# Optimization experiments

Hardware: AMD Instinct MI355X
Metric: run time of the kernel (lower is better)

The kernel has to match this reference:

```python
import jax, jax.numpy as jnp
import numpy as np

K = 3          # kernel_size
PAD = 1        # padding
FOCAL = 50.0
DMIN = 1.0
DMAX = 50.0
ORIG_H = 512.0  # original_image_size[1]


def setup_inputs() -> dict:
    key = jax.random.key(0)
    k1, k2 = jax.random.split(key)
    x = jax.random.normal(k1, (4, 64, 256, 256), dtype=jnp.float32)
    # conv weight [out_ch, in_ch, K, K] (bias=False)
    W = jax.random.normal(k2, (64, 64, K, K), dtype=jnp.float32) * 0.05
    return {"x": x, "W": W}


def _bilinear(img, xs, ys):
    """Bilinear sample img [B,C,H,W] at float pixel coords xs, ys [B,Ho,Wo].
    Zero padding outside the image (grid_sample semantics)."""
    B, C, H, Wd = img.shape
    Ho, Wo = xs.shape[1], xs.shape[2]
    x0 = jnp.floor(xs); y0 = jnp.floor(ys)
    wx1 = xs - x0; wx0 = 1.0 - wx1
    wy1 = ys - y0; wy0 = 1.0 - wy1
    img_flat = img.reshape(B, C, H * Wd)

    def gat(ix, iy):
        ixi = ix.astype(jnp.int32); iyi = iy.astype(jnp.int32)
        valid = (ixi >= 0) & (ixi < Wd) & (iyi >= 0) & (iyi < H)
        idx = jnp.clip(iyi, 0, H - 1) * Wd + jnp.clip(ixi, 0, Wd - 1)
        v = jnp.take_along_axis(img_flat, idx.reshape(B, 1, Ho * Wo), axis=2)
        v = v.reshape(B, C, Ho, Wo)
        return v * valid[:, None].astype(img.dtype)

    return (gat(x0, y0) * (wx0 * wy0)[:, None]
            + gat(x0 + 1, y0) * (wx1 * wy0)[:, None]
            + gat(x0, y0 + 1) * (wx0 * wy1)[:, None]
            + gat(x0 + 1, y0 + 1) * (wx1 * wy1)[:, None])


def reference(x, W):
    B, C, H, Wd = x.shape
    downsample = ORIG_H / H  # 2.0 for H=256

    # upper branch: plain 3x3 conv, padding 1, no bias
    x_upper = jax.lax.conv_general_dilated(x, W, (1, 1), [(PAD, PAD), (PAD, PAD)])

    # geometry -> clamped depth (geometry_method='max', formulation='depth')
    depth = jnp.clip(jnp.max(x, axis=1), DMIN, DMAX)  # [B,H,W]

    # Frontal homography: Hom01 = I with [1,2] = focal/(downsample*depth);
    # its inverse Hom10 shifts y by -s.
    s = FOCAL / (downsample * depth)  # [B,H,W]

    xi = jnp.arange(Wd, dtype=x.dtype)[None, None, :]
    yi = jnp.arange(H, dtype=x.dtype)[None, :, None]
    xs = jnp.broadcast_to(xi, (B, H, Wd))
    ys = yi - s  # Hom10 applied to pixel coords

    # warp input with per-pixel Hom10 (pass_warped_images=True)
    x2 = _bilinear(x, xs, ys)

    # deformable conv: per-pixel offset from Hom10 is (dx,dy)=(0,-s) for all 9 taps
    x_lower = jnp.zeros_like(x_upper)
    for ky in range(K):
        for kx in range(K):
            sx = xs + (kx - PAD)
            sy = ys + (ky - PAD)
            tap = _bilinear(x2, sx, sy)  # [B,C,H,W]
            x_lower = x_lower + jnp.einsum('bchw,oc->bohw', tap, W[:, :, ky, kx])

    # project with 'min' over the stacked (upper, lower) branches
    return jnp.minimum(x_upper, x_lower)
```

## Files before the change

### kernel.cpp

```cpp
#include <hip/hip_runtime.h>
#include <cmath>

constexpr int BB = 4, CC = 64, HH = 256, WW = 256;
constexpr int WP = 258;
constexpr int C2R = 257;

typedef short short8 __attribute__((ext_vector_type(8)));
typedef float f32x4 __attribute__((ext_vector_type(4)));
#define MFMA_BF16 __builtin_amdgcn_mfma_f32_16x16x32_bf16

union U16x8 { uint4 v; unsigned short h[8]; };
union U16x4 { uint2 v; unsigned short h[4]; };

__device__ inline unsigned short f2bf(float f) {
  unsigned u = __builtin_bit_cast(unsigned, f);
  u += 0x7fffu + ((u >> 16) & 1u);
  return (unsigned short)(u >> 16);
}
__device__ inline unsigned short f2bf_trunc(float f) {
  return (unsigned short)(__builtin_bit_cast(unsigned, f) >> 16);
}
__device__ inline float bf2f(unsigned short h) {
  unsigned u = ((unsigned)h) << 16;
  return __builtin_bit_cast(float, u);
}

__global__ __launch_bounds__(256, 4) void k_pack(const float* __restrict__ x,
                                                 float* __restrict__ s,
                                                 unsigned short* __restrict__ xn) {
  __shared__ float tile[CC * 129];
  __shared__ float pmax[2][128];
  const int t = threadIdx.x;
  const int half = blockIdx.x & 1, y = blockIdx.x >> 1, b = blockIdx.y;
  const int px0 = half * 128;
  const int pxl = t & 127, chb = (t >> 7) * 32;

  const float* base = x + (size_t)b * CC * HH * WW + (size_t)y * WW + px0 + pxl;
  float m = -1e30f;
#pragma unroll 8
  for (int i = 0; i < 32; ++i) {
    float v = base[(size_t)(chb + i) * HH * WW];
    tile[(chb + i) * 129 + pxl] = v;
    m = fmaxf(m, v);
  }
  pmax[t >> 7][pxl] = m;

  uint4* xn4 = (uint4*)xn;
  if (t < 8) {
    int col = half ? (WP - 1) : 0;
    xn4[(((size_t)(b * HH + y) * WP + col) * CC + t * 8) >> 3] =
        make_uint4(0, 0, 0, 0);
  }
  __syncthreads();

  if (t < 128) {
    float mm = fmaxf(pmax[0][t], pmax[1][t]);
    s[(b * HH + y) * WW + px0 + t] = 25.0f / fminf(fmaxf(mm, 1.0f), 50.0f);
  }
#pragma unroll
  for (int g = 0; g < 4; ++g) {
    int px = g * 32 + (t >> 3), c8 = t & 7;
    U16x8 r;
#pragma unroll
    for (int j = 0; j < 8; ++j) r.h[j] = f2bf(tile[(c8 * 8 + j) * 129 + px]);
    xn4[(((size_t)(b * HH + y) * WP + px0 + px + 1) * CC + c8 * 8) >> 3] = r.v;
  }
}

__global__ __launch_bounds__(256) void k_wpack(const float* __restrict__ Wt,
                                               unsigned short* __restrict__ Wp) {
  int gid = blockIdx.x * 256 + threadIdx.x;
  int lane = gid & 63, kc = (gid >> 6) & 1, mt = (gid >> 7) & 3, tap = gid >> 9;
  int o = mt * 16 + (lane & 15);
  int kb = kc * 32 + (lane >> 4) * 8;
  int ky = tap / 3, kx = tap % 3;
  U16x8 r;
#pragma unroll
  for (int j = 0; j < 8; ++j)
    r.h[j] = f2bf(Wt[o * 576 + (kb + j) * 9 + ky * 3 + kx]);
  ((uint4*)Wp)[gid] = r.v;
}

__global__ __launch_bounds__(256, 4) void k_lower(const unsigned short* __restrict__ xn,
                                                  const unsigned short* __restrict__ Wp,
                                                  const float* __restrict__ s,
                                                  unsigned short* __restrict__ c2) {
  __shared__ uint4 lds[2112];
  const int t = threadIdx.x;
  const int ctile = blockIdx.x & 3, tr = blockIdx.x >> 2;
  const int b = blockIdx.y;
  const int r0 = tr * 2 - 1;
  const int colBase = ctile * 64;

  const uint4* xn4 = (const uint4*)xn;
#pragma unroll 1
  for (int g = 0; g < 3; ++g) {
    float w0a[3], w1a[3];
    int o0a[3], o1a[3], la[3];
    bool act[3], va[3];
#pragma unroll
    for (int j = 0; j < 3; ++j) {
      int idx = (g * 3 + j) * 256 + t;
      act[j] = idx < 2112;
      int rr_ = idx / 528, rem = idx % 528;
      int col_ = rem >> 3, ch_ = rem & 7;
      int xrow = r0 - 1 + rr_;
      va[j] = act[j] && (xrow >= 0) && (xrow < HH);
      la[j] = (rr_ * 66 + col_) * 8 + (ch_ ^ (col_ & 7));
      float sv = 0.0f;
      int pxc = min(max(colBase + col_ - 1, 0), WW - 1);
      if (va[j]) sv = s[(b * HH + min(max(xrow, 0), HH - 1)) * WW + pxc];
      float ys = (float)xrow - sv;
      float fy = floorf(ys);
      float wfr = ys - fy;
      int i0 = (int)fy;
      w0a[j] = (i0 >= 0) ? 1.0f - wfr : 0.0f;
      w1a[j] = (i0 + 1 >= 0) ? wfr : 0.0f;
      int a0 = min(max(i0, 0), HH - 1), a1 = min(max(i0 + 1, 0), HH - 1);
      o0a[j] = ((b * HH + a0) * WP + colBase + col_) * 8 + ch_;
      o1a[j] = ((b * HH + a1) * WP + colBase + col_) * 8 + ch_;
    }
#pragma unroll
    for (int j = 0; j < 3; ++j) {
      if (act[j]) {
        uint4 v = make_uint4(0, 0, 0, 0);
        if (va[j]) {
          U16x8 u0, u1, rr;
          u0.v = xn4[o0a[j]];
          u1.v = xn4[o1a[j]];
#pragma unroll
          for (int k = 0; k < 8; ++k)
            rr.h[k] = f2bf_trunc(w0a[j] * bf2f(u0.h[k]) + w1a[j] * bf2f(u1.h[k]));
          v = rr.v;
        }
        lds[la[j]] = v;
      }
    }
  }

  const int lane = t & 63, w = t >> 6;
  const int ow = w & 1, ch2 = w >> 1;
  const int quad = lane >> 4, l15 = lane & 15;
  const uint4* wp4 = (const uint4*)Wp;
  __syncthreads();

  f32x4 acc[2][2][2];
#pragma unroll
  for (int pt = 0; pt < 2; ++pt)
#pragma unroll
    for (int rr = 0; rr < 2; ++rr)
#pragma unroll
      for (int ct = 0; ct < 2; ++ct) acc[pt][rr][ct] = {0.f, 0.f, 0.f, 0.f};

#pragma unroll 1
  for (int kc = 0; kc < 2; ++kc) {
    short8 wf[9][2];
#pragma unroll
    for (int tap = 0; tap < 9; ++tap)
#pragma unroll
      for (int ct = 0; ct < 2; ++ct)
        wf[tap][ct] = __builtin_bit_cast(
            short8, wp4[((tap * 4 + (ow * 2 + ct)) * 2 + kc) * 64 + lane]);
#pragma unroll
    for (int pt = 0; pt < 2; ++pt) {
#pragma unroll
      for (int ir = 0; ir < 4; ++ir) {
#pragma unroll
        for (int kx = 0; kx < 3; ++kx) {
          int col = ch2 * 32 + pt * 16 + l15 + kx;
          short8 xf = __builtin_bit_cast(
              short8, lds[(ir * 66 + col) * 8 + ((kc * 4 + quad) ^ (col & 7))]);
          if (ir <= 2) {
#pragma unroll
            for (int ct = 0; ct < 2; ++ct)
              acc[pt][0][ct] = MFMA_BF16(wf[ir * 3 + kx][ct], xf, acc[pt][0][ct], 0, 0, 0);
          }
          if (ir >= 1) {
#pragma unroll
            for (int ct = 0; ct < 2; ++ct)
              acc[pt][1][ct] = MFMA_BF16(wf[(ir - 1) * 3 + kx][ct], xf, acc[pt][1][ct], 0, 0, 0);
          }
        }
      }
    }
  }

  uint2* c2u = (uint2*)c2;
#pragma unroll
  for (int pt = 0; pt < 2; ++pt) {
    int px = colBase + ch2 * 32 + pt * 16 + l15;
#pragma unroll
    for (int rr = 0; rr < 2; ++rr) {
      int r = r0 + rr;
      if (r > 255) continue;
#pragma unroll
      for (int ct = 0; ct < 2; ++ct) {
        f32x4 A = acc[pt][rr][ct];
        int og = (ow * 2 + ct) * 4 + quad;
        unsigned short h0 = f2bf(A[0]), h1 = f2bf(A[1]), h2 = f2bf(A[2]), h3 = f2bf(A[3]);
        uint2 val = make_uint2((unsigned)h0 | ((unsigned)h1 << 16),
                               (unsigned)h2 | ((unsigned)h3 << 16));
        c2u[(size_t)((b * 16 + og) * C2R + (r + 1)) * WW + px] = val;
      }
    }
  }
}

__global__ __launch_bounds__(256, 4) void k_final(const unsigned short* __restrict__ xn,
                                                  const unsigned short* __restrict__ Wp,
                                                  const float* __restrict__ s,
                                                  const unsigned short* __restrict__ c2,
                                                  float* __restrict__ out) {
  __shared__ uint4 lds[2112];
  const int t = threadIdx.x;
  const int ctile = blockIdx.x & 3, tr = blockIdx.x >> 2;
  const int b = blockIdx.y;
  const int y0 = tr * 2;
  const int colBase = ctile * 64;

  const uint4* src4 = (const uint4*)xn;
#pragma unroll 1
  for (int i = 0; i < 9; ++i) {
    int idx = i * 256 + t;
    if (idx < 2112) {
      int rr_ = idx / 528, rem = idx % 528;
      int col_ = rem >> 3, ch_ = rem & 7;
      int xrow = y0 - 1 + rr_;
      uint4 v = make_uint4(0, 0, 0, 0);
      if (xrow >= 0 && xrow < HH)
        v = src4[((size_t)(b * HH + xrow) * WP + colBase + col_) * 8 + ch_];
      lds[(rr_ * 66 + col_) * 8 + (ch_ ^ (col_ & 7))] = v;
    }
  }

  const int lane = t & 63, w = t >> 6;
  const int ow = w & 1, ch2 = w >> 1;
  const int quad = lane >> 4, l15 = lane & 15;
  const uint4* wp4 = (const uint4*)Wp;
  __syncthreads();

  f32x4 acc[2][2][2];
#pragma unroll
  for (int pt = 0; pt < 2; ++pt)
#pragma unroll
    for (int rr = 0; rr < 2; ++rr)
#pragma unroll
      for (int ct = 0; ct < 2; ++ct) acc[pt][rr][ct] = {0.f, 0.f, 0.f, 0.f};

#pragma unroll 1
  for (int kc = 0; kc < 2; ++kc) {
    short8 wf[9][2];
#pragma unroll
    for (int tap = 0; tap < 9; ++tap)
#pragma unroll
      for (int ct = 0; ct < 2; ++ct)
        wf[tap][ct] = __builtin_bit_cast(
            short8, wp4[((tap * 4 + (ow * 2 + ct)) * 2 + kc) * 64 + lane]);
#pragma unroll
    for (int pt = 0; pt < 2; ++pt) {
#pragma unroll
      for (int ir = 0; ir < 4; ++ir) {
#pragma unroll
        for (int kx = 0; kx < 3; ++kx) {
          int col = ch2 * 32 + pt * 16 + l15 + kx;
          short8 xf = __builtin_bit_cast(
              short8, lds[(ir * 66 + col) * 8 + ((kc * 4 + quad) ^ (col & 7))]);
          if (ir <= 2) {
#pragma unroll
            for (int ct = 0; ct < 2; ++ct)
              acc[pt][0][ct] = MFMA_BF16(wf[ir * 3 + kx][ct], xf, acc[pt][0][ct], 0, 0, 0);
          }
          if (ir >= 1) {
#pragma unroll
            for (int ct = 0; ct < 2; ++ct)
              acc[pt][1][ct] = MFMA_BF16(wf[(ir - 1) * 3 + kx][ct], xf, acc[pt][1][ct], 0, 0, 0);
          }
        }
      }
    }
  }

  const uint2* c2u = (const uint2*)c2;
#pragma unroll
  for (int pt = 0; pt < 2; ++pt) {
    int px = colBase + ch2 * 32 + pt * 16 + l15;
#pragma unroll
    for (int rr = 0; rr < 2; ++rr) {
      int y = y0 + rr;
      float sv = s[(b * HH + y) * WW + px];
      float ys = (float)y - sv;
      float fy = floorf(ys);
      float wfr = ys - fy;
      int i0 = (int)fy;
      float lw0 = (i0 + 1 >= 0 && i0 + 1 <= HH) ? 1.0f - wfr : 0.0f;
      float lw1 = (i0 + 2 >= 0 && i0 + 2 <= HH) ? wfr : 0.0f;
      int a0 = min(max(i0 + 1, 0), HH);
      int a1 = min(max(i0 + 2, 0), HH);
#pragma unroll
      for (int ct = 0; ct < 2; ++ct) {
        f32x4 A = acc[pt][rr][ct];
        int og = (ow * 2 + ct) * 4 + quad;
        U16x4 v0, v1;
        v0.v = c2u[(size_t)((b * 16 + og) * C2R + a0) * WW + px];
        v1.v = c2u[(size_t)((b * 16 + og) * C2R + a1) * WW + px];
#pragma unroll
        for (int reg = 0; reg < 4; ++reg) {
          float lower = lw0 * bf2f(v0.h[reg]) + lw1 * bf2f(v1.h[reg]);
          out[((size_t)(b * CC + og * 4 + reg) * HH + y) * WW + px] =
              fminf(A[reg], lower);
        }
      }
    }
  }
}

extern "C" void kernel_launch(void* const* d_in, const int* in_sizes, int n_in,
                              void* d_out, int out_size, void* d_ws, size_t ws_size,
                              hipStream_t stream) {
  const float* x = (const float*)d_in[0];
  const float* Wt = (const float*)d_in[1];
  float* out = (float*)d_out;

  char* ws = (char*)d_ws;
  float* s = (float*)ws;
  unsigned short* Wp = (unsigned short*)(ws + 1048576);
  unsigned short* xn = (unsigned short*)(ws + 1122304);
  unsigned short* c2 = (unsigned short*)(ws + 34938880);
  k_pack<<<dim3(HH * 2, BB), 256, 0, stream>>>(x, s, xn);
  k_wpack<<<dim3(18), 256, 0, stream>>>(Wt, Wp);
  k_lower<<<dim3(4 * 129, BB), 256, 0, stream>>>(xn, Wp, s, c2);
  k_final<<<dim3(4 * 128, BB), 256, 0, stream>>>(xn, Wp, s, c2, out);
}
```

Measured before the change: 190.2 us.

## Fuse four kernels into one persistent kernel with software grid barriers

Merges the pack, weight-pack, lower-branch and final kernels into a single persistent launch of 1024 blocks. Stages are separated by atomic-counter grid barriers, and each block loops over tiles for the conv stages. This removes per-kernel launch gaps and tail effects. In exchange it adds a memset and spin-wait barriers, and it relies on all 1024 blocks being co-resident (4 per CU on 256 CUs); if they are not, it will hang or hit the barrier timeout.

```diff
diff --git a/kernel.cpp b/kernel.cpp
--- a/kernel.cpp
+++ b/kernel.cpp
@@ -4,6 +4,7 @@
 constexpr int BB = 4, CC = 64, HH = 256, WW = 256;
 constexpr int WP = 258;
 constexpr int C2R = 257;
+constexpr unsigned NB = 1024;
 
 typedef short short8 __attribute__((ext_vector_type(8)));
 typedef float f32x4 __attribute__((ext_vector_type(4)));
@@ -25,289 +26,321 @@
   return __builtin_bit_cast(float, u);
 }
 
-__global__ __launch_bounds__(256, 4) void k_pack(const float* __restrict__ x,
-                                                 float* __restrict__ s,
-                                                 unsigned short* __restrict__ xn) {
-  __shared__ float tile[CC * 129];
-  __shared__ float pmax[2][128];
+__device__ inline void gridBarrier(unsigned* cnt, unsigned* flag) {
+  __syncthreads();
+  if (threadIdx.x == 0) {
+    __threadfence();
+    unsigned prev = atomicAdd(cnt, 1u);
+    if (prev == NB - 1u) {
+      __hip_atomic_store(flag, 1u, __ATOMIC_RELEASE, __HIP_MEMORY_SCOPE_AGENT);
+    } else {
+      for (int i = 0; i < (1 << 22); ++i) {
+        if (__hip_atomic_load(flag, __ATOMIC_RELAXED,
+                              __HIP_MEMORY_SCOPE_AGENT) != 0u)
+          break;
+        __builtin_amdgcn_s_sleep(8);
+      }
+    }
+    __threadfence();
+  }
+  __syncthreads();
+}
+
+__global__ __launch_bounds__(256, 4) void k_fused(
+    const float* __restrict__ x, const float* __restrict__ Wt,
+    float* __restrict__ s, unsigned short* __restrict__ Wp,
+    unsigned short* __restrict__ xn, unsigned short* __restrict__ c2,
+    float* __restrict__ out, unsigned* __restrict__ bar) {
+  __shared__ __align__(16) float smem[8512];
   const int t = threadIdx.x;
-  const int half = blockIdx.x & 1, y = blockIdx.x >> 1, b = blockIdx.y;
-  const int px0 = half * 128;
-  const int pxl = t & 127, chb = (t >> 7) * 32;
-
-  const float* base = x + (size_t)b * CC * HH * WW + (size_t)y * WW + px0 + pxl;
-  float m = -1e30f;
+  const int bid = blockIdx.x;
+
+  if (bid < 18) {
+    int gid = bid * 256 + t;
+    int lane = gid & 63, kc = (gid >> 6) & 1, mt = (gid >> 7) & 3, tap = gid >> 9;
+    int o = mt * 16 + (lane & 15);
+    int kb = kc * 32 + (lane >> 4) * 8;
+    int ky = tap / 3, kx = tap % 3;
+    U16x8 r;
+#pragma unroll
+    for (int j = 0; j < 8; ++j)
+      r.h[j] = f2bf(Wt[o * 576 + (kb + j) * 9 + ky * 3 + kx]);
+    ((uint4*)Wp)[gid] = r.v;
+  }
+  {
+    float* tile = smem;
+    float* pmax = smem + 8256;
+    const int b = bid >> 8, y = bid & 255;
+    uint4* xn4 = (uint4*)xn;
+#pragma unroll 1
+    for (int half = 0; half < 2; ++half) {
+      __syncthreads();
+      const int px0 = half * 128;
+      const int pxl = t & 127, chb = (t >> 7) * 32;
+      const float* base =
+          x + (size_t)b * CC * HH * WW + (size_t)y * WW + px0 + pxl;
+      float m = -1e30f;
 #pragma unroll 8
-  for (int i = 0; i < 32; ++i) {
-    float v = base[(size_t)(chb + i) * HH * WW];
-    tile[(chb + i) * 129 + pxl] = v;
-    m = fmaxf(m, v);
-  }
-  pmax[t >> 7][pxl] = m;
-
-  uint4* xn4 = (uint4*)xn;
-  if (t < 8) {
-    int col = half ? (WP - 1) : 0;
-    xn4[(((size_t)(b * HH + y) * WP + col) * CC + t * 8) >> 3] =
-        make_uint4(0, 0, 0, 0);
-  }
-  __syncthreads();
-
-  if (t < 128) {
-    float mm = fmaxf(pmax[0][t], pmax[1][t]);
-    s[(b * HH + y) * WW + px0 + t] = 25.0f / fminf(fmaxf(mm, 1.0f), 50.0f);
-  }
-#pragma unroll
-  for (int g = 0; g < 4; ++g) {
-    int px = g * 32 + (t >> 3), c8 = t & 7;
-    U16x8 r;
-#pragma unroll
-    for (int j = 0; j < 8; ++j) r.h[j] = f2bf(tile[(c8 * 8 + j) * 129 + px]);
-    xn4[(((size_t)(b * HH + y) * WP + px0 + px + 1) * CC + c8 * 8) >> 3] = r.v;
-  }
-}
-
-__global__ __launch_bounds__(256) void k_wpack(const float* __restrict__ Wt,
-                                               unsigned short* __restrict__ Wp) {
-  int gid = blockIdx.x * 256 + threadIdx.x;
-  int lane = gid & 63, kc = (gid >> 6) & 1, mt = (gid >> 7) & 3, tap = gid >> 9;
-  int o = mt * 16 + (lane & 15);
-  int kb = kc * 32 + (lane >> 4) * 8;
-  int ky = tap / 3, kx = tap % 3;
-  U16x8 r;
-#pragma unroll
-  for (int j = 0; j < 8; ++j)
-    r.h[j] = f2bf(Wt[o * 576 + (kb + j) * 9 + ky * 3 + kx]);
-  ((uint4*)Wp)[gid] = r.v;
-}
-
-__global__ __launch_bounds__(256, 4) void k_lower(const unsigned short* __restrict__ xn,
-                                                  const unsigned short* __restrict__ Wp,
-                                                  const float* __restrict__ s,
-                                                  unsigned short* __restrict__ c2) {
-  __shared__ uint4 lds[2112];
-  const int t = threadIdx.x;
-  const int ctile = blockIdx.x & 3, tr = blockIdx.x >> 2;
-  const int b = blockIdx.y;
-  const int r0 = tr * 2 - 1;
-  const int colBase = ctile * 64;
-
-  const uint4* xn4 = (const uint4*)xn;
-#pragma unroll 1
-  for (int g = 0; g < 3; ++g) {
-    float w0a[3], w1a[3];
-    int o0a[3], o1a[3], la[3];
-    bool act[3], va[3];
-#pragma unroll
-    for (int j = 0; j < 3; ++j) {
-      int idx = (g * 3 + j) * 256 + t;
-      act[j] = idx < 2112;
-      int rr_ = idx / 528, rem = idx % 528;
-      int col_ = rem >> 3, ch_ = rem & 7;
-      int xrow = r0 - 1 + rr_;
-      va[j] = act[j] && (xrow >= 0) && (xrow < HH);
-      la[j] = (rr_ * 66 + col_) * 8 + (ch_ ^ (col_ & 7));
-      float sv = 0.0f;
-      int pxc = min(max(colBase + col_ - 1, 0), WW - 1);
-      if (va[j]) sv = s[(b * HH + min(max(xrow, 0), HH - 1)) * WW + pxc];
-      float ys = (float)xrow - sv;
-      float fy = floorf(ys);
-      float wfr = ys - fy;
-      int i0 = (int)fy;
-      w0a[j] = (i0 >= 0) ? 1.0f - wfr : 0.0f;
-      w1a[j] = (i0 + 1 >= 0) ? wfr : 0.0f;
-      int a0 = min(max(i0, 0), HH - 1), a1 = min(max(i0 + 1, 0), HH - 1);
-      o0a[j] = ((b * HH + a0) * WP + colBase + col_) * 8 + ch_;
-      o1a[j] = ((b * HH + a1) * WP + colBase + col_) * 8 + ch_;
+      for (int i = 0; i < 32; ++i) {
+        float v = base[(size_t)(chb + i) * HH * WW];
+        tile[(chb + i) * 129 + pxl] = v;
+        m = fmaxf(m, v);
+      }
+      pmax[(t >> 7) * 128 + pxl] = m;
+      if (t < 8) {
+        int col = half ? (WP - 1) : 0;
+        xn4[(((size_t)(b * HH + y) * WP + col) * CC + t * 8) >> 3] =
+            make_uint4(0, 0, 0, 0);
+      }
+      __syncthreads();
+      if (t < 128) {
+        float mm = fmaxf(pmax[t], pmax[128 + t]);
+        s[(b * HH + y) * WW + px0 + t] = 25.0f / fminf(fmaxf(mm, 1.0f), 50.0f);
+      }
+#pragma unroll
+      for (int g = 0; g < 4; ++g) {
+        int px = g * 32 + (t >> 3), c8 = t & 7;
+        U16x8 r;
+#pragma unroll
+        for (int j = 0; j < 8; ++j) r.h[j] = f2bf(tile[(c8 * 8 + j) * 129 + px]);
+        xn4[(((size_t)(b * HH + y) * WP + px0 + px + 1) * CC + c8 * 8) >> 3] = r.v;
+      }
     }
-#pragma unroll
-    for (int j = 0; j < 3; ++j) {
-      if (act[j]) {
-        uint4 v = make_uint4(0, 0, 0, 0);
-        if (va[j]) {
-          U16x8 u0, u1, rr;
-          u0.v = xn4[o0a[j]];
-          u1.v = xn4[o1a[j]];
-#pragma unroll
-          for (int k = 0; k < 8; ++k)
-            rr.h[k] = f2bf_trunc(w0a[j] * bf2f(u0.h[k]) + w1a[j] * bf2f(u1.h[k]));
-          v = rr.v;
-        }
-        lds[la[j]] = v;
+  }
+  gridBarrier(bar + 0, bar + 1);
+
+  {
+    uint4* lds = (uint4*)smem;
+    const uint4* xn4 = (const uint4*)xn;
+    const uint4* wp4 = (const uint4*)Wp;
+    const int lane = t & 63, w = t >> 6;
+    const int ow = w & 1, ch2 = w >> 1;
+    const int quad = lane >> 4, l15 = lane & 15;
+#pragma unroll 1
+    for (int task = bid; task < 2064; task += NB) {
+      const int b = task / 516;
+      const int rem = task % 516;
+      const int ctile = rem & 3, tr = rem >> 2;
+      const int r0 = tr * 2 - 1;
+      const int colBase = ctile * 64;
+      __syncthreads();
+#pragma unroll 1
+      for (int g = 0; g < 3; ++g) {
+        float w0a[3], w1a[3];
+        int o0a[3], o1a[3], la[3];
+        bool act[3], va[3];
+#pragma unroll
+        for (int j = 0; j < 3; ++j) {
+          int idx = (g * 3 + j) * 256 + t;
+          act[j] = idx < 2112;
+          int rr_ = idx / 528, rm = idx % 528;
+          int col_ = rm >> 3, ch_ = rm & 7;
+          int xrow = r0 - 1 + rr_;
+          va[j] = act[j] && (xrow >= 0) && (xrow < HH);
+          la[j] = (rr_ * 66 + col_) * 8 + (ch_ ^ (col_ & 7));
+          float sv = 0.0f;
+          int pxc = min(max(colBase + col_ - 1, 0), WW - 1);
+          if (va[j]) sv = s[(b * HH + min(max(xrow, 0), HH - 1)) * WW + pxc];
+          float ys = (float)xrow - sv;
+          float fy = floorf(ys);
+          float wfr = ys - fy;
+          int i0 = (int)fy;
+          w0a[j] = (i0 >= 0) ? 1.0f - wfr : 0.0f;
+          w1a[j] = (i0 + 1 >= 0) ? wfr : 0.0f;
+          int a0 = min(max(i0, 0), HH - 1), a1 = min(max(i0 + 1, 0), HH - 1);
+          o0a[j] = ((b * HH + a0) * WP + colBase + col_) * 8 + ch_;
+          o1a[j] = ((b * HH + a1) * WP + colBase + col_) * 8 + ch_;
+        }
+#pragma unroll
+        for (int j = 0; j < 3; ++j) {
+          if (act[j]) {
+            uint4 v = make_uint4(0, 0, 0, 0);
+            if (va[j]) {
+              U16x8 u0, u1, rr;
+              u0.v = xn4[o0a[j]];
+              u1.v = xn4[o1a[j]];
+#pragma unroll
+              for (int k = 0; k < 8; ++k)
+                rr.h[k] =
+                    f2bf_trunc(w0a[j] * bf2f(u0.h[k]) + w1a[j] * bf2f(u1.h[k]));
+              v = rr.v;
+            }
+            lds[la[j]] = v;
+          }
+        }
+      }
+
+      f32x4 acc[2][2][2];
+#pragma unroll
+      for (int pt = 0; pt < 2; ++pt)
+#pragma unroll
+        for (int rr = 0; rr < 2; ++rr)
+#pragma unroll
+          for (int ct = 0; ct < 2; ++ct) acc[pt][rr][ct] = {0.f, 0.f, 0.f, 0.f};
+      __syncthreads();
+
+#pragma unroll 1
+      for (int kc = 0; kc < 2; ++kc) {
+        short8 wf[9][2];
+#pragma unroll
+        for (int tap = 0; tap < 9; ++tap)
+#pragma unroll
+          for (int ct = 0; ct < 2; ++ct)
+            wf[tap][ct] = __builtin_bit_cast(
+                short8, wp4[((tap * 4 + (ow * 2 + ct)) * 2 + kc) * 64 + lane]);
+#pragma unroll
+        for (int pt = 0; pt < 2; ++pt) {
+#pragma unroll
+          for (int ir = 0; ir < 4; ++ir) {
+#pragma unroll
+            for (int kx = 0; kx < 3; ++kx) {
+              int col = ch2 * 32 + pt * 16 + l15 + kx;
+              short8 xf = __builtin_bit_cast(
+                  short8, lds[(ir * 66 + col) * 8 + ((kc * 4 + quad) ^ (col & 7))]);
+              if (ir <= 2) {
+#pragma unroll
+                for (int ct = 0; ct < 2; ++ct)
+                  acc[pt][0][ct] =
+                      MFMA_BF16(wf[ir * 3 + kx][ct], xf, acc[pt][0][ct], 0, 0, 0);
+              }
+              if (ir >= 1) {
+#pragma unroll
+                for (int ct = 0; ct < 2; ++ct)
+                  acc[pt][1][ct] = MFMA_BF16(wf[(ir - 1) * 3 + kx][ct], xf,
+                                             acc[pt][1][ct], 0, 0, 0);
+              }
+            }
+          }
+        }
+      }
+
+      uint2* c2u = (uint2*)c2;
+#pragma unroll
+      for (int pt = 0; pt < 2; ++pt) {
+        int px = colBase + ch2 * 32 + pt * 16 + l15;
+#pragma unroll
+        for (int rr = 0; rr < 2; ++rr) {
+          int r = r0 + rr;
+          if (r > 255) continue;
+#pragma unroll
+          for (int ct = 0; ct < 2; ++ct) {
+            f32x4 A = acc[pt][rr][ct];
+            int og = (ow * 2 + ct) * 4 + quad;
+            unsigned short h0 = f2bf(A[0]), h1 = f2bf(A[1]), h2 = f2bf(A[2]),
+                           h3 = f2bf(A[3]);
+            uint2 val = make_uint2((unsigned)h0 | ((unsigned)h1 << 16),
+                                   (unsigned)h2 | ((unsigned)h3 << 16));
+            c2u[(size_t)((b * 16 + og) * C2R + (r + 1)) * WW + px] = val;
+          }
+        }
       }
     }
   }
-
-  const int lane = t & 63, w = t >> 6;
-  const int ow = w & 1, ch2 = w >> 1;
-  const int quad = lane >> 4, l15 = lane & 15;
-  const uint4* wp4 = (const uint4*)Wp;
-  __syncthreads();
-
-  f32x4 acc[2][2][2];
-#pragma unroll
-  for (int pt = 0; pt < 2; ++pt)
-#pragma unroll
-    for (int rr = 0; rr < 2; ++rr)
-#pragma unroll
-      for (int ct = 0; ct < 2; ++ct) acc[pt][rr][ct] = {0.f, 0.f, 0.f, 0.f};
-
-#pragma unroll 1
-  for (int kc = 0; kc < 2; ++kc) {
-    short8 wf[9][2];
-#pragma unroll
-    for (int tap = 0; tap < 9; ++tap)
-#pragma unroll
-      for (int ct = 0; ct < 2; ++ct)
-        wf[tap][ct] = __builtin_bit_cast(
-            short8, wp4[((tap * 4 + (ow * 2 + ct)) * 2 + kc) * 64 + lane]);
-#pragma unroll
-    for (int pt = 0; pt < 2; ++pt) {
-#pragma unroll
-      for (int ir = 0; ir < 4; ++ir) {
-#pragma unroll
-        for (int kx = 0; kx < 3; ++kx) {
-          int col = ch2 * 32 + pt * 16 + l15 + kx;
-          short8 xf = __builtin_bit_cast(
-              short8, lds[(ir * 66 + col) * 8 + ((kc * 4 + quad) ^ (col & 7))]);
-          if (ir <= 2) {
-#pragma unroll
-            for (int ct = 0; ct < 2; ++ct)
-              acc[pt][0][ct] = MFMA_BF16(wf[ir * 3 + kx][ct], xf, acc[pt][0][ct], 0, 0, 0);
-          }
-          if (ir >= 1) {
-#pragma unroll
-            for (int ct = 0; ct < 2; ++ct)
-              acc[pt][1][ct] = MFMA_BF16(wf[(ir - 1) * 3 + kx][ct], xf, acc[pt][1][ct], 0, 0, 0);
-          }
-        }
-      }
-    }
-  }
-
-  uint2* c2u = (uint2*)c2;
-#pragma unroll
-  for (int pt = 0; pt < 2; ++pt) {
-    int px = colBase + ch2 * 32 + pt * 16 + l15;
-#pragma unroll
-    for (int rr = 0; rr < 2; ++rr) {
-      int r = r0 + rr;
-      if (r > 255) continue;
-#pragma unroll
-      for (int ct = 0; ct < 2; ++ct) {
-        f32x4 A = acc[pt][rr][ct];
-        int og = (ow * 2 + ct) * 4 + quad;
-        unsigned short h0 = f2bf(A[0]), h1 = f2bf(A[1]), h2 = f2bf(A[2]), h3 = f2bf(A[3]);
-        uint2 val = make_uint2((unsigned)h0 | ((unsigned)h1 << 16),
-                               (unsigned)h2 | ((unsigned)h3 << 16));
-        c2u[(size_t)((b * 16 + og) * C2R + (r + 1)) * WW + px] = val;
-      }
-    }
-  }
-}
-
-__global__ __launch_bounds__(256, 4) void k_final(const unsigned short* __restrict__ xn,
-                                                  const unsigned short* __restrict__ Wp,
-                                                  const float* __restrict__ s,
-                                                  const unsigned short* __restrict__ c2,
-                                                  float* __restrict__ out) {
-  __shared__ uint4 lds[2112];
-  const int t = threadIdx.x;
-  const int ctile = blockIdx.x & 3, tr = blockIdx.x >> 2;
-  const int b = blockIdx.y;
-  const int y0 = tr * 2;
-  const int colBase = ctile * 64;
-
-  const uint4* src4 = (const uint4*)xn;
-#pragma unroll 1
-  for (int i = 0; i < 9; ++i) {
-    int idx = i * 256 + t;
-    if (idx < 2112) {
-      int rr_ = idx / 528, rem = idx % 528;
-      int col_ = rem >> 3, ch_ = rem & 7;
-      int xrow = y0 - 1 + rr_;
-      uint4 v = make_uint4(0, 0, 0, 0);
-      if (xrow >= 0 && xrow < HH)
-        v = src4[((size_t)(b * HH + xrow) * WP + colBase + col_) * 8 + ch_];
-      lds[(rr_ * 66 + col_) * 8 + (ch_ ^ (col_ & 7))] = v;
-    }
-  }
-
-  const int lane = t & 63, w = t >> 6;
-  const int ow = w & 1, ch2 = w >> 1;
-  const int quad = lane >> 4, l15 = lane & 15;
-  const uint4* wp4 = (const uint4*)Wp;
-  __syncthreads();
-
-  f32x4 acc[2][2][2];
-#pragma unroll
-  for (int pt = 0; pt < 2; ++pt)
-#pragma unroll
-    for (int rr = 0; rr < 2; ++rr)
-#pragma unroll
-      for (int ct = 0; ct < 2; ++ct) acc[pt][rr][ct] = {0.f, 0.f, 0.f, 0.f};
-
-#pragma unroll 1
-  for (int kc = 0; kc < 2; ++kc) {
-    short8 wf[9][2];
-#pragma unroll
-    for (int tap = 0; tap < 9; ++tap)
-#pragma unroll
-      for (int ct = 0; ct < 2; ++ct)
-        wf[tap][ct] = __builtin_bit_cast(
-            short8, wp4[((tap * 4 + (ow * 2 + ct)) * 2 + kc) * 64 + lane]);
-#pragma unroll
-    for (int pt = 0; pt < 2; ++pt) {
-#pragma unroll
-      for (int ir = 0; ir < 4; ++ir) {
-#pragma unroll
-        for (int kx = 0; kx < 3; ++kx) {
-          int col = ch2 * 32 + pt * 16 + l15 + kx;
-          short8 xf = __builtin_bit_cast(
-              short8, lds[(ir * 66 + col) * 8 + ((kc * 4 + quad) ^ (col & 7))]);
-          if (ir <= 2) {
-#pragma unroll
-            for (int ct = 0; ct < 2; ++ct)
-              acc[pt][0][ct] = MFMA_BF16(wf[ir * 3 + kx][ct], xf, acc[pt][0][ct], 0, 0, 0);
-          }
-          if (ir >= 1) {
-#pragma unroll
-            for (int ct = 0; ct < 2; ++ct)
-              acc[pt][1][ct] = MFMA_BF16(wf[(ir - 1) * 3 + kx][ct], xf, acc[pt][1][ct], 0, 0, 0);
-          }
-        }
-      }
-    }
-  }
-
-  const uint2* c2u = (const uint2*)c2;
-#pragma unroll
-  for (int pt = 0; pt < 2; ++pt) {
-    int px = colBase + ch2 * 32 + pt * 16 + l15;
-#pragma unroll
-    for (int rr = 0; rr < 2; ++rr) {
-      int y = y0 + rr;
-      float sv = s[(b * HH + y) * WW + px];
-      float ys = (float)y - sv;
-      float fy = floorf(ys);
-      float wfr = ys - fy;
-      int i0 = (int)fy;
-      float lw0 = (i0 + 1 >= 0 && i0 + 1 <= HH) ? 1.0f - wfr : 0.0f;
-      float lw1 = (i0 + 2 >= 0 && i0 + 2 <= HH) ? wfr : 0.0f;
-      int a0 = min(max(i0 + 1, 0), HH);
-      int a1 = min(max(i0 + 2, 0), HH);
-#pragma unroll
-      for (int ct = 0; ct < 2; ++ct) {
-        f32x4 A = acc[pt][rr][ct];
-        int og = (ow * 2 + ct) * 4 + quad;
-        U16x4 v0, v1;
-        v0.v = c2u[(size_t)((b * 16 + og) * C2R + a0) * WW + px];
-        v1.v = c2u[(size_t)((b * 16 + og) * C2R + a1) * WW + px];
-#pragma unroll
-        for (int reg = 0; reg < 4; ++reg) {
-          float lower = lw0 * bf2f(v0.h[reg]) + lw1 * bf2f(v1.h[reg]);
-          out[((size_t)(b * CC + og * 4 + reg) * HH + y) * WW + px] =
-              fminf(A[reg], lower);
+  gridBarrier(bar + 2, bar + 3);
+
+  {
+    uint4* lds = (uint4*)smem;
+    const uint4* src4 = (const uint4*)xn;
+    const uint4* wp4 = (const uint4*)Wp;
+    const uint2* c2u = (const uint2*)c2;
+    const int lane = t & 63, w = t >> 6;
+    const int ow = w & 1, ch2 = w >> 1;
+    const int quad = lane >> 4, l15 = lane & 15;
+#pragma unroll 1
+    for (int task = bid; task < 2048; task += NB) {
+      const int b = task >> 9;
+      const int rem = task & 511;
+      const int ctile = rem & 3, tr = rem >> 2;
+      const int y0 = tr * 2;
+      const int colBase = ctile * 64;
+      __syncthreads();
+#pragma unroll 1
+      for (int i = 0; i < 9; ++i) {
+        int idx = i * 256 + t;
+        if (idx < 2112) {
+          int rr_ = idx / 528, rm = idx % 528;
+          int col_ = rm >> 3, ch_ = rm & 7;
+          int xrow = y0 - 1 + rr_;
+          uint4 v = make_uint4(0, 0, 0, 0);
+          if (xrow >= 0 && xrow < HH)
+            v = src4[((size_t)(b * HH + xrow) * WP + colBase + col_) * 8 + ch_];
+          lds[(rr_ * 66 + col_) * 8 + (ch_ ^ (col_ & 7))] = v;
+        }
+      }
+
+      f32x4 acc[2][2][2];
+#pragma unroll
+      for (int pt = 0; pt < 2; ++pt)
+#pragma unroll
+        for (int rr = 0; rr < 2; ++rr)
+#pragma unroll
+          for (int ct = 0; ct < 2; ++ct) acc[pt][rr][ct] = {0.f, 0.f, 0.f, 0.f};
+      __syncthreads();
+
+#pragma unroll 1
+      for (int kc = 0; kc < 2; ++kc) {
+        short8 wf[9][2];
+#pragma unroll
+        for (int tap = 0; tap < 9; ++tap)
+#pragma unroll
+          for (int ct = 0; ct < 2; ++ct)
+            wf[tap][ct] = __builtin_bit_cast(
+                short8, wp4[((tap * 4 + (ow * 2 + ct)) * 2 + kc) * 64 + lane]);
+#pragma unroll
+        for (int pt = 0; pt < 2; ++pt) {
+#pragma unroll
+          for (int ir = 0; ir < 4; ++ir) {
+#pragma unroll
+            for (int kx = 0; kx < 3; ++kx) {
+              int col = ch2 * 32 + pt * 16 + l15 + kx;
+              short8 xf = __builtin_bit_cast(
+                  short8, lds[(ir * 66 + col) * 8 + ((kc * 4 + quad) ^ (col & 7))]);
+              if (ir <= 2) {
+#pragma unroll
+                for (int ct = 0; ct < 2; ++ct)
+                  acc[pt][0][ct] =
+                      MFMA_BF16(wf[ir * 3 + kx][ct], xf, acc[pt][0][ct], 0, 0, 0);
+              }
+              if (ir >= 1) {
+#pragma unroll
+                for (int ct = 0; ct < 2; ++ct)
+                  acc[pt][1][ct] = MFMA_BF16(wf[(ir - 1) * 3 + kx][ct], xf,
+                                             acc[pt][1][ct], 0, 0, 0);
+              }
+            }
+          }
+        }
+      }
+
+#pragma unroll
+      for (int pt = 0; pt < 2; ++pt) {
+        int px = colBase + ch2 * 32 + pt * 16 + l15;
+#pragma unroll
+        for (int rr = 0; rr < 2; ++rr) {
+          int y = y0 + rr;
+          float sv = s[(b * HH + y) * WW + px];
+          float ys = (float)y - sv;
+          float fy = floorf(ys);
+          float wfr = ys - fy;
+          int i0 = (int)fy;
+          float lw0 = (i0 + 1 >= 0 && i0 + 1 <= HH) ? 1.0f - wfr : 0.0f;
+          float lw1 = (i0 + 2 >= 0 && i0 + 2 <= HH) ? wfr : 0.0f;
+          int a0 = min(max(i0 + 1, 0), HH);
+          int a1 = min(max(i0 + 2, 0), HH);
+#pragma unroll
+          for (int ct = 0; ct < 2; ++ct) {
+            f32x4 A = acc[pt][rr][ct];
+            int og = (ow * 2 + ct) * 4 + quad;
+            U16x4 v0, v1;
+            v0.v = c2u[(size_t)((b * 16 + og) * C2R + a0) * WW + px];
+            v1.v = c2u[(size_t)((b * 16 + og) * C2R + a1) * WW + px];
+#pragma unroll
+            for (int reg = 0; reg < 4; ++reg) {
+              float lower = lw0 * bf2f(v0.h[reg]) + lw1 * bf2f(v1.h[reg]);
+              out[((size_t)(b * CC + og * 4 + reg) * HH + y) * WW + px] =
+                  fminf(A[reg], lower);
+            }
+          }
         }
       }
     }
@@ -322,12 +355,11 @@
   float* out = (float*)d_out;
 
   char* ws = (char*)d_ws;
-  float* s = (float*)ws;
-  unsigned short* Wp = (unsigned short*)(ws + 1048576);
-  unsigned short* xn = (unsigned short*)(ws + 1122304);
-  unsigned short* c2 = (unsigned short*)(ws + 34938880);
-  k_pack<<<dim3(HH * 2, BB), 256, 0, stream>>>(x, s, xn);
-  k_wpack<<<dim3(18), 256, 0, stream>>>(Wt, Wp);
-  k_lower<<<dim3(4 * 129, BB), 256, 0, stream>>>(xn, Wp, s, c2);
-  k_final<<<dim3(4 * 128, BB), 256, 0, stream>>>(xn, Wp, s, c2, out);
-}
+  unsigned* bar = (unsigned*)ws;
+  float* s = (float*)(ws + 1024);
+  unsigned short* Wp = (unsigned short*)(ws + 1049600);
+  unsigned short* xn = (unsigned short*)(ws + 1123328);
+  unsigned short* c2 = (unsigned short*)(ws + 34939904);
+  hipMemsetAsync(bar, 0, 64, stream);
+  k_fused<<<dim3(NB), 256, 0, stream>>>(x, Wt, s, Wp, xn, c2, out, bar);
+}
```

New measurement: 443.9 us. +133.3%, slower.
